# Kernel tuning notes

Measured on AMD Instinct MI355X. Metric: run time of the kernel, lower is better.

## Reference

```python
import jax, jax.numpy as jnp
import numpy as np

B, IN_E, IN_I, D = 4096, 4096, 4096, 2048
IN_BR = 8192
BS = IN_BR // D  # block size = 4
K_E, K_I = 50, 1
E_TO_I = 50.0
BN_EPS = 1e-5


def setup_inputs() -> dict:
    key = jax.random.key(0)
    ks = jax.random.split(key, 8)
    # fan-in uniform init like nn.Linear (kaiming-uniform bound ~ 1/sqrt(in))
    def linw(k, out_f, in_f):
        b = 1.0 / np.sqrt(in_f)
        return jax.random.uniform(k, (out_f, in_f), jnp.float32, -b, b)
    return {
        "excitatory_input": jax.random.normal(ks[0], (B, IN_E), jnp.float32),
        "inhibitory_input": jax.random.normal(ks[1], (B, IN_I), jnp.float32),
        "dendrite_branch_outputs": jax.random.uniform(ks[2], (B, IN_BR), jnp.float32),
        "w_exc": linw(ks[3], D, IN_E),
        "w_inh": linw(ks[4], D, IN_I),
        "w_block": linw(ks[5], D, IN_BR),
        "bn_gamma": jnp.ones((D,), jnp.float32),
        "bn_beta": jnp.zeros((D,), jnp.float32),
    }


def _topk_linear(x, w, k):
    # keep the k largest weights per output row, zero the rest, then matmul
    idx = jax.lax.top_k(w, k)[1]                          # [D, k]
    mask = jnp.zeros_like(w).at[jnp.arange(w.shape[0])[:, None], idx].set(1.0)
    return x @ (w * mask).T                               # [B, D]


def _block_linear(x, w):
    # block-diagonal mask: row c uses columns [c*BS, (c+1)*BS)
    out_f = w.shape[0]
    wb = w.reshape(out_f, out_f, BS)[jnp.arange(out_f), jnp.arange(out_f)]  # [D, BS]
    xb = x.reshape(x.shape[0], out_f, BS)                                   # [B, D, BS]
    return jnp.einsum('bds,ds->bd', xb, wb)


def reference(excitatory_input, inhibitory_input, dendrite_branch_outputs,
              w_exc, w_inh, w_block, bn_gamma, bn_beta):
    dendrite_excitation = _topk_linear(excitatory_input, w_exc, K_E)
    dendrite_inhibition = _topk_linear(inhibitory_input, w_inh, K_I)
    dendrite_depolarization = _block_linear(dendrite_branch_outputs, w_block)
    total_excitatory = dendrite_excitation + dendrite_depolarization
    # neuron_type == 'excitatory'
    act = total_excitatory - E_TO_I * dendrite_inhibition
    # BatchNorm1d, training mode: batch stats, biased variance
    mean = jnp.mean(act, axis=0)
    var = jnp.var(act, axis=0)
    act = (act - mean) * jax.lax.rsqrt(var + BN_EPS) * bn_gamma + bn_beta
    return jax.nn.sigmoid(act)
```

## Files before the change

kernel.cpp:

```cpp
#include <hip/hip_runtime.h>
#include <hip/hip_fp16.h>

#define B_     4096
#define INE_   4096
#define INBR_  8192
#define D_     2048
#define KE_    50
#define KPAD_  52
#define CAP_   512
#define NSL_   4

__device__ __forceinline__ unsigned packh2(float a, float b) {
  __half2 h = __floats2half2_rn(a, b);
  return __builtin_bit_cast(unsigned, h);
}
__device__ __forceinline__ float2 unpackh2(unsigned u) {
  __half2 h = __builtin_bit_cast(__half2, u);
  return __half22float2(h);
}

__device__ void topk_body(const float* __restrict__ W, int row, int k, int kpad,
                          float hi, float t0, float vscale,
                          uint4* __restrict__ muT,
                          unsigned* __restrict__ out_off, float* __restrict__ out_val)
{
  const int t = threadIdx.x;
  const float* wr = W + (size_t)row * INE_;

  __shared__ float cval[CAP_];
  __shared__ int   ccol[CAP_];
  __shared__ int   scnt;
  __shared__ int   red[4];

  float thr = t0;
  int M = 0;
  for (int attempt = 0; attempt < 8; ++attempt) {
    int local = 0;
    #pragma unroll
    for (int j = 0; j < 4; ++j) {
      float4 w4 = *reinterpret_cast<const float4*>(wr + 4 * (t + 256 * j));
      local += (w4.x > thr) + (w4.y > thr) + (w4.z > thr) + (w4.w > thr);
    }
    #pragma unroll
    for (int off = 32; off > 0; off >>= 1) local += __shfl_down(local, off);
    if ((t & 63) == 0) red[t >> 6] = local;
    __syncthreads();
    M = red[0] + red[1] + red[2] + red[3];
    __syncthreads();
    if (M >= k && M <= CAP_) break;
    if (M < k) thr = hi - (hi - thr) * 4.0f;
    else       thr = hi - (hi - thr) * 0.5f;
  }

  if (t == 0) scnt = 0;
  __syncthreads();
  #pragma unroll
  for (int j = 0; j < 4; ++j) {
    int cbase = 4 * (t + 256 * j);
    float4 w4 = *reinterpret_cast<const float4*>(wr + cbase);
    float wv[4] = {w4.x, w4.y, w4.z, w4.w};
    #pragma unroll
    for (int q = 0; q < 4; ++q) {
      if (wv[q] > thr) {
        int pp = atomicAdd(&scnt, 1);
        if (pp < CAP_) { cval[pp] = wv[q]; ccol[pp] = cbase + q; }
      }
    }
  }
  __syncthreads();
  M = scnt < CAP_ ? scnt : CAP_;

  for (int i = t; i < M; i += 256) {
    float wi = cval[i]; int ci = ccol[i];
    int rank = 0;
    for (int m = 0; m < M; ++m) {
      float wm = cval[m]; int cm = ccol[m];
      rank += (wm > wi || (wm == wi && cm < ci)) ? 1 : 0;
    }
    if (rank < k) {
      unsigned c = (unsigned)ci;
      unsigned off = ((c >> 2) << 3) | ((c & 3u) << 13);
      if (kpad == 1) {
        out_off[row] = off;
        out_val[row] = wi * vscale;
      } else {
        char* rec = (char*)muT + ((size_t)(rank >> 2) * D_ + row) * 16;
        reinterpret_cast<unsigned short*>(rec)[rank & 3] = (unsigned short)off;
        reinterpret_cast<__half*>(rec)[4 + (rank & 3)] =
            __float2half_rn(wi * vscale);
      }
    }
  }
  if (kpad > 1 && t < kpad - k) {
    int slot = k + t;
    char* rec = (char*)muT + ((size_t)(slot >> 2) * D_ + row) * 16;
    reinterpret_cast<unsigned short*>(rec)[slot & 3] = 0;
    reinterpret_cast<__half*>(rec)[4 + (slot & 3)] = __float2half_rn(0.0f);
  }
}

__global__ __launch_bounds__(256) void prep_kernel(
    const float* __restrict__ wexc, const float* __restrict__ winh,
    const float* __restrict__ wblk,
    uint4* __restrict__ muT,
    unsigned* __restrict__ so_inh, float* __restrict__ vi_inh,
    float* __restrict__ wdiag)
{
  const int bid = blockIdx.x;
  const float hi = 0.015625f;
  if (bid < 2048) {
    topk_body(wexc, bid, KE_, KPAD_, hi, hi * (1.0f - 200.0f / 4096.0f), 1.0f,
              muT, nullptr, nullptr);
  } else if (bid < 4096) {
    topk_body(winh, bid - 2048, 1, 1, hi, hi * (1.0f - 48.0f / 4096.0f), -50.0f,
              nullptr, so_inh, vi_inh);
  } else {
    const int t = threadIdx.x;
    #pragma unroll
    for (int j = 0; j < 8; ++j) {
      int d = t + 256 * j;
      float4 w = *reinterpret_cast<const float4*>(wblk + (size_t)d * (INBR_ + 4));
      reinterpret_cast<float4*>(wdiag)[d] = w;
    }
  }
}

__device__ __forceinline__ uint2 ld8(const char* ldsb, unsigned off) {
  return *reinterpret_cast<const uint2*>(ldsb + off);
}

#define FMA4(R, G, WV) do {                                                \
    float2 f0 = unpackh2((G).x), f1 = unpackh2((G).y);                     \
    acc[R][0] = fmaf(f0.x, (WV), acc[R][0]);                               \
    acc[R][1] = fmaf(f0.y, (WV), acc[R][1]);                               \
    acc[R][2] = fmaf(f1.x, (WV), acc[R][2]);                               \
    acc[R][3] = fmaf(f1.y, (WV), acc[R][3]);                               \
  } while (0)

__device__ __forceinline__ void do_br(float (&acc)[4][4], int t, int b0,
                                      const float* __restrict__ xbr,
                                      const float* __restrict__ wdiag) {
  #pragma unroll
  for (int r = 0; r < 4; ++r) {
    const int d = t + 512 * r;
    float4 wb4 = reinterpret_cast<const float4*>(wdiag)[d];
    #pragma unroll
    for (int b = 0; b < 4; ++b) {
      float4 xb4 = *reinterpret_cast<const float4*>(
          xbr + (size_t)(b0 + b) * INBR_ + 4 * d);
      acc[r][b] += xb4.x * wb4.x + xb4.y * wb4.y + xb4.z * wb4.z + xb4.w * wb4.w;
    }
  }
}

__global__ __launch_bounds__(512, 4) void fused_ei(
    const float* __restrict__ xe, const float* __restrict__ xi,
    const float* __restrict__ xbr, const float* __restrict__ wdiag,
    const uint4* __restrict__ muT,
    const unsigned* __restrict__ so_inh, const float* __restrict__ vi_inh,
    float* __restrict__ act, float* __restrict__ sums_p,
    float* __restrict__ sumsq_p)
{
  __shared__ unsigned xs[8192];
  const int t  = threadIdx.x;
  const int b0 = blockIdx.x * 4;
  const int p  = t & 1;
  const int Q  = t >> 1;

  float acc[4][4];
  #pragma unroll
  for (int r = 0; r < 4; ++r)
    #pragma unroll
    for (int b = 0; b < 4; ++b) acc[r][b] = 0.0f;

  const char* ldsb = reinterpret_cast<const char*>(xs);
  const bool brf = (blockIdx.x & 1);

  if (brf) do_br(acc, t, b0, xbr, wdiag);

  {
    const float* r0p = xe + (size_t)(b0 + 2 * p)     * INE_;
    const float* r1p = xe + (size_t)(b0 + 2 * p + 1) * INE_;
    #pragma unroll
    for (int m = 0; m < 4; ++m) {
      int c0 = 4 * Q + 1024 * m;
      float4 fa = *reinterpret_cast<const float4*>(r0p + c0);
      float4 fb = *reinterpret_cast<const float4*>(r1p + c0);
      int wb = 2 * (Q + 256 * m) + p;
      xs[wb]        = packh2(fa.x, fb.x);
      xs[wb + 2048] = packh2(fa.y, fb.y);
      xs[wb + 4096] = packh2(fa.z, fb.z);
      xs[wb + 6144] = packh2(fa.w, fb.w);
    }
  }

  float4 xia[4];
  {
    const float* xr0 = xi + (size_t)(b0 + 2 * p) * INE_;
    #pragma unroll
    for (int m = 0; m < 4; ++m)
      xia[m] = *reinterpret_cast<const float4*>(xr0 + 4 * Q + 1024 * m);
  }
  unsigned oi[4]; float viv[4];
  #pragma unroll
  for (int r = 0; r < 4; ++r) {
    oi[r]  = so_inh[t + 512 * r];
    viv[r] = vi_inh[t + 512 * r];
  }
  __syncthreads();

  for (int ii = 0; ii < KPAD_ / 4; ++ii) {
    uint4 m[4];
    #pragma unroll
    for (int r = 0; r < 4; ++r) m[r] = muT[ii * D_ + t + 512 * r];
    #pragma unroll
    for (int half = 0; half < 2; ++half) {
      uint2 g[2][4];
      #pragma unroll
      for (int rr = 0; rr < 2; ++rr) {
        const int r = 2 * half + rr;
        g[rr][0] = ld8(ldsb, m[r].x & 0xFFFFu);
        g[rr][1] = ld8(ldsb, m[r].x >> 16);
        g[rr][2] = ld8(ldsb, m[r].y & 0xFFFFu);
        g[rr][3] = ld8(ldsb, m[r].y >> 16);
      }
      #pragma unroll
      for (int rr = 0; rr < 2; ++rr) {
        const int r = 2 * half + rr;
        float2 vA = unpackh2(m[r].z);
        float2 vB = unpackh2(m[r].w);
        FMA4(r, g[rr][0], vA.x);
        FMA4(r, g[rr][1], vA.y);
        FMA4(r, g[rr][2], vB.x);
        FMA4(r, g[rr][3], vB.y);
      }
    }
  }
  __syncthreads();

  {
    const float* xr1 = xi + (size_t)(b0 + 2 * p + 1) * INE_;
    #pragma unroll
    for (int m = 0; m < 4; ++m) {
      int c0 = 4 * Q + 1024 * m;
      float4 fb = *reinterpret_cast<const float4*>(xr1 + c0);
      int wb = 2 * (Q + 256 * m) + p;
      xs[wb]        = packh2(xia[m].x, fb.x);
      xs[wb + 2048] = packh2(xia[m].y, fb.y);
      xs[wb + 4096] = packh2(xia[m].z, fb.z);
      xs[wb + 6144] = packh2(xia[m].w, fb.w);
    }
  }
  __syncthreads();

  {
    uint2 gi[4];
    #pragma unroll
    for (int r = 0; r < 4; ++r) gi[r] = ld8(ldsb, oi[r]);
    #pragma unroll
    for (int r = 0; r < 4; ++r) FMA4(r, gi[r], viv[r]);
  }

  if (!brf) do_br(acc, t, b0, xbr, wdiag);

  const int slice = blockIdx.x & (NSL_ - 1);
  #pragma unroll
  for (int r = 0; r < 4; ++r) {
    const int d = t + 512 * r;
    float s = 0.0f, s2 = 0.0f;
    #pragma unroll
    for (int b = 0; b < 4; ++b) {
      float a = acc[r][b];
      act[(size_t)(b0 + b) * D_ + d] = a;
      s += a;
      s2 = fmaf(a, a, s2);
    }
    atomicAdd(&sums_p[slice * D_ + d], s);
    atomicAdd(&sumsq_p[slice * D_ + d], s2);
  }
}

__global__ __launch_bounds__(256) void tail_kernel(
    const float* __restrict__ act, float* __restrict__ out,
    const float* __restrict__ sums_p, const float* __restrict__ sumsq_p,
    const float* __restrict__ gamma, const float* __restrict__ beta)
{
  __shared__ float scsh[2 * D_];
  const int tid = threadIdx.x;
  #pragma unroll
  for (int j = 0; j < 8; ++j) {
    int d = tid + 256 * j;
    float s = 0.0f, s2 = 0.0f;
    #pragma unroll
    for (int sl = 0; sl < NSL_; ++sl) {
      s  += sums_p[sl * D_ + d];
      s2 += sumsq_p[sl * D_ + d];
    }
    float mean = s  * (1.0f / B_);
    float var  = s2 * (1.0f / B_) - mean * mean;
    float rstd = rsqrtf(var + 1e-5f);
    float sc   = gamma[d] * rstd;
    scsh[2 * d]     = sc;
    scsh[2 * d + 1] = fmaf(-mean, sc, beta[d]);
  }
  __syncthreads();

  const int r0 = blockIdx.x * 8;
  for (int rr = 0; rr < 8; ++rr) {
    const float4* ap = reinterpret_cast<const float4*>(act + (size_t)(r0 + rr) * D_);
    float4*       op = reinterpret_cast<float4*>(out + (size_t)(r0 + rr) * D_);
    #pragma unroll
    for (int i2 = 0; i2 < 2; ++i2) {
      int i = tid + 256 * i2;
      float4 a = ap[i];
      const float4* sp = reinterpret_cast<const float4*>(scsh + 8 * i);
      float4 s0 = sp[0];
      float4 s1 = sp[1];
      float z0 = fmaf(a.x, s0.x, s0.y);
      float z1 = fmaf(a.y, s0.z, s0.w);
      float z2 = fmaf(a.z, s1.x, s1.y);
      float z3 = fmaf(a.w, s1.z, s1.w);
      float4 o;
      o.x = 1.0f / (1.0f + __expf(-z0));
      o.y = 1.0f / (1.0f + __expf(-z1));
      o.z = 1.0f / (1.0f + __expf(-z2));
      o.w = 1.0f / (1.0f + __expf(-z3));
      op[i] = o;
    }
  }
}

extern "C" void kernel_launch(void* const* d_in, const int* in_sizes, int n_in,
                              void* d_out, int out_size, void* d_ws, size_t ws_size,
                              hipStream_t stream) {
  const float* xe    = (const float*)d_in[0];
  const float* xi    = (const float*)d_in[1];
  const float* xbr   = (const float*)d_in[2];
  const float* wexc  = (const float*)d_in[3];
  const float* winh  = (const float*)d_in[4];
  const float* wblk  = (const float*)d_in[5];
  const float* gamma = (const float*)d_in[6];
  const float* beta  = (const float*)d_in[7];
  float* out = (float*)d_out;

  char* ws = (char*)d_ws;
  uint4*    muT     = (uint4*)   (ws + 0);
  unsigned* so_inh  = (unsigned*)(ws + 425984);
  float*    vi_inh  = (float*)   (ws + 434176);
  float*    wdiag   = (float*)   (ws + 442368);
  float*    sums_p  = (float*)   (ws + 475136);
  float*    sumsq_p = (float*)   (ws + 507904);
  float*    act     = (float*)   (ws + 1048576);

  hipMemsetAsync(sums_p, 0, 2 * NSL_ * D_ * sizeof(float), stream);

  prep_kernel<<<dim3(4097), dim3(256), 0, stream>>>(
      wexc, winh, wblk, muT, so_inh, vi_inh, wdiag);
  fused_ei<<<dim3(B_ / 4), dim3(512), 0, stream>>>(
      xe, xi, xbr, wdiag, muT, so_inh, vi_inh, act, sums_p, sumsq_p);
  tail_kernel<<<dim3(512), dim3(256), 0, stream>>>(
      act, out, sums_p, sumsq_p, gamma, beta);
}
```

Before: 125.8 us.

## Gather inhibitory inputs directly, drop second LDS stage, store activations as fp16

The inhibitory top-1 path now gathers the single needed input column per output straight from global memory, instead of staging the whole inhibitory input into shared memory. This removes two barriers and a full 4 KB-per-row read of the inhibitory input. The branch dot-product is moved to the end with no per-block alternation. The intermediate activation buffer is written and read as fp16 rather than fp32, halving traffic between the fused kernel and the tail kernel, at the cost of some precision before batch normalisation. The scattered gathers are uncoalesced but small.

```diff
diff --git a/kernel.cpp b/kernel.cpp
--- a/kernel.cpp
+++ b/kernel.cpp
@@ -79,11 +79,11 @@
     }
     if (rank < k) {
       unsigned c = (unsigned)ci;
-      unsigned off = ((c >> 2) << 3) | ((c & 3u) << 13);
       if (kpad == 1) {
-        out_off[row] = off;
+        out_off[row] = c;
         out_val[row] = wi * vscale;
       } else {
+        unsigned off = ((c >> 2) << 3) | ((c & 3u) << 13);
         char* rec = (char*)muT + ((size_t)(rank >> 2) * D_ + row) * 16;
         reinterpret_cast<unsigned short*>(rec)[rank & 3] = (unsigned short)off;
         reinterpret_cast<__half*>(rec)[4 + (rank & 3)] =
@@ -137,28 +137,12 @@
     acc[R][3] = fmaf(f1.y, (WV), acc[R][3]);                               \
   } while (0)
 
-__device__ __forceinline__ void do_br(float (&acc)[4][4], int t, int b0,
-                                      const float* __restrict__ xbr,
-                                      const float* __restrict__ wdiag) {
-  #pragma unroll
-  for (int r = 0; r < 4; ++r) {
-    const int d = t + 512 * r;
-    float4 wb4 = reinterpret_cast<const float4*>(wdiag)[d];
-    #pragma unroll
-    for (int b = 0; b < 4; ++b) {
-      float4 xb4 = *reinterpret_cast<const float4*>(
-          xbr + (size_t)(b0 + b) * INBR_ + 4 * d);
-      acc[r][b] += xb4.x * wb4.x + xb4.y * wb4.y + xb4.z * wb4.z + xb4.w * wb4.w;
-    }
-  }
-}
-
 __global__ __launch_bounds__(512, 4) void fused_ei(
     const float* __restrict__ xe, const float* __restrict__ xi,
     const float* __restrict__ xbr, const float* __restrict__ wdiag,
     const uint4* __restrict__ muT,
     const unsigned* __restrict__ so_inh, const float* __restrict__ vi_inh,
-    float* __restrict__ act, float* __restrict__ sums_p,
+    __half* __restrict__ act_h, float* __restrict__ sums_p,
     float* __restrict__ sumsq_p)
 {
   __shared__ unsigned xs[8192];
@@ -174,9 +158,6 @@
     for (int b = 0; b < 4; ++b) acc[r][b] = 0.0f;
 
   const char* ldsb = reinterpret_cast<const char*>(xs);
-  const bool brf = (blockIdx.x & 1);
-
-  if (brf) do_br(acc, t, b0, xbr, wdiag);
 
   {
     const float* r0p = xe + (size_t)(b0 + 2 * p)     * INE_;
@@ -194,18 +175,20 @@
     }
   }
 
-  float4 xia[4];
-  {
-    const float* xr0 = xi + (size_t)(b0 + 2 * p) * INE_;
-    #pragma unroll
-    for (int m = 0; m < 4; ++m)
-      xia[m] = *reinterpret_cast<const float4*>(xr0 + 4 * Q + 1024 * m);
-  }
-  unsigned oi[4]; float viv[4];
+  unsigned ci[4]; float viv[4];
   #pragma unroll
   for (int r = 0; r < 4; ++r) {
-    oi[r]  = so_inh[t + 512 * r];
+    ci[r]  = so_inh[t + 512 * r];
     viv[r] = vi_inh[t + 512 * r];
+  }
+  float xg0[4], xg1[4], xg2[4], xg3[4];
+  #pragma unroll
+  for (int b = 0; b < 4; ++b) {
+    const float* xrow = xi + (size_t)(b0 + b) * INE_;
+    xg0[b] = xrow[ci[0]];
+    xg1[b] = xrow[ci[1]];
+    xg2[b] = xrow[ci[2]];
+    xg3[b] = xrow[ci[3]];
   }
   __syncthreads();
 
@@ -236,32 +219,26 @@
       }
     }
   }
-  __syncthreads();
-
-  {
-    const float* xr1 = xi + (size_t)(b0 + 2 * p + 1) * INE_;
-    #pragma unroll
-    for (int m = 0; m < 4; ++m) {
-      int c0 = 4 * Q + 1024 * m;
-      float4 fb = *reinterpret_cast<const float4*>(xr1 + c0);
-      int wb = 2 * (Q + 256 * m) + p;
-      xs[wb]        = packh2(xia[m].x, fb.x);
-      xs[wb + 2048] = packh2(xia[m].y, fb.y);
-      xs[wb + 4096] = packh2(xia[m].z, fb.z);
-      xs[wb + 6144] = packh2(xia[m].w, fb.w);
-    }
-  }
-  __syncthreads();
-
-  {
-    uint2 gi[4];
-    #pragma unroll
-    for (int r = 0; r < 4; ++r) gi[r] = ld8(ldsb, oi[r]);
-    #pragma unroll
-    for (int r = 0; r < 4; ++r) FMA4(r, gi[r], viv[r]);
-  }
-
-  if (!brf) do_br(acc, t, b0, xbr, wdiag);
+
+  #pragma unroll
+  for (int b = 0; b < 4; ++b) {
+    acc[0][b] = fmaf(xg0[b], viv[0], acc[0][b]);
+    acc[1][b] = fmaf(xg1[b], viv[1], acc[1][b]);
+    acc[2][b] = fmaf(xg2[b], viv[2], acc[2][b]);
+    acc[3][b] = fmaf(xg3[b], viv[3], acc[3][b]);
+  }
+
+  #pragma unroll
+  for (int r = 0; r < 4; ++r) {
+    const int d = t + 512 * r;
+    float4 wb4 = reinterpret_cast<const float4*>(wdiag)[d];
+    #pragma unroll
+    for (int b = 0; b < 4; ++b) {
+      float4 xb4 = *reinterpret_cast<const float4*>(
+          xbr + (size_t)(b0 + b) * INBR_ + 4 * d);
+      acc[r][b] += xb4.x * wb4.x + xb4.y * wb4.y + xb4.z * wb4.z + xb4.w * wb4.w;
+    }
+  }
 
   const int slice = blockIdx.x & (NSL_ - 1);
   #pragma unroll
@@ -271,7 +248,7 @@
     #pragma unroll
     for (int b = 0; b < 4; ++b) {
       float a = acc[r][b];
-      act[(size_t)(b0 + b) * D_ + d] = a;
+      act_h[(size_t)(b0 + b) * D_ + d] = __float2half_rn(a);
       s += a;
       s2 = fmaf(a, a, s2);
     }
@@ -281,7 +258,7 @@
 }
 
 __global__ __launch_bounds__(256) void tail_kernel(
-    const float* __restrict__ act, float* __restrict__ out,
+    const __half* __restrict__ act_h, float* __restrict__ out,
     const float* __restrict__ sums_p, const float* __restrict__ sumsq_p,
     const float* __restrict__ gamma, const float* __restrict__ beta)
 {
@@ -307,19 +284,21 @@
 
   const int r0 = blockIdx.x * 8;
   for (int rr = 0; rr < 8; ++rr) {
-    const float4* ap = reinterpret_cast<const float4*>(act + (size_t)(r0 + rr) * D_);
-    float4*       op = reinterpret_cast<float4*>(out + (size_t)(r0 + rr) * D_);
+    const uint2* ap = reinterpret_cast<const uint2*>(act_h + (size_t)(r0 + rr) * D_);
+    float4*      op = reinterpret_cast<float4*>(out + (size_t)(r0 + rr) * D_);
     #pragma unroll
     for (int i2 = 0; i2 < 2; ++i2) {
       int i = tid + 256 * i2;
-      float4 a = ap[i];
+      uint2 aw = ap[i];
+      float2 f0 = unpackh2(aw.x);
+      float2 f1 = unpackh2(aw.y);
       const float4* sp = reinterpret_cast<const float4*>(scsh + 8 * i);
       float4 s0 = sp[0];
       float4 s1 = sp[1];
-      float z0 = fmaf(a.x, s0.x, s0.y);
-      float z1 = fmaf(a.y, s0.z, s0.w);
-      float z2 = fmaf(a.z, s1.x, s1.y);
-      float z3 = fmaf(a.w, s1.z, s1.w);
+      float z0 = fmaf(f0.x, s0.x, s0.y);
+      float z1 = fmaf(f0.y, s0.z, s0.w);
+      float z2 = fmaf(f1.x, s1.x, s1.y);
+      float z3 = fmaf(f1.y, s1.z, s1.w);
       float4 o;
       o.x = 1.0f / (1.0f + __expf(-z0));
       o.y = 1.0f / (1.0f + __expf(-z1));
@@ -350,14 +329,14 @@
   float*    wdiag   = (float*)   (ws + 442368);
   float*    sums_p  = (float*)   (ws + 475136);
   float*    sumsq_p = (float*)   (ws + 507904);
-  float*    act     = (float*)   (ws + 1048576);
+  __half*   act_h   = (__half*)  (ws + 1048576);
 
   hipMemsetAsync(sums_p, 0, 2 * NSL_ * D_ * sizeof(float), stream);
 
   prep_kernel<<<dim3(4097), dim3(256), 0, stream>>>(
       wexc, winh, wblk, muT, so_inh, vi_inh, wdiag);
   fused_ei<<<dim3(B_ / 4), dim3(512), 0, stream>>>(
-      xe, xi, xbr, wdiag, muT, so_inh, vi_inh, act, sums_p, sumsq_p);
+      xe, xi, xbr, wdiag, muT, so_inh, vi_inh, act_h, sums_p, sumsq_p);
   tail_kernel<<<dim3(512), dim3(256), 0, stream>>>(
-      act, out, sums_p, sumsq_p, gamma, beta);
-}
+      act_h, out, sums_p, sumsq_p, gamma, beta);
+}
```

Measured after the change: 124.6 us, median of 3. Within noise of the previous version (-0.9%).
